# Kernel tuning notes

Measured on AMD Instinct MI355X. Metric: run time of the kernel, lower is better.

Reference implementation:

```python
import jax, jax.numpy as jnp
import numpy as np


def pairwise_distance(x):
    # x: [B,N,F] -> squared euclidean distance matrix [B,N,N]
    sq = jnp.sum(x * x, axis=-1)
    d = sq[:, :, None] + sq[:, None, :] - 2.0 * jnp.einsum('bnd,bmd->bnm', x, x)
    return jnp.maximum(d, 0.0)


def knn_adjacency(dist, k):
    # keep the k nearest neighbors of each point (binary adjacency)
    B, N, _ = dist.shape
    idx = jax.lax.top_k(-dist, k)[1]  # [B,N,k]
    A = jnp.zeros((B, N, N), dist.dtype)
    return A.at[jnp.arange(B)[:, None, None], jnp.arange(N)[None, :, None], idx].set(1.0)


def get_laplacian(A):
    # normalized graph Laplacian L = I - D^{-1/2} A D^{-1/2}
    d = jnp.sum(A, axis=-1)
    dinv = jnp.where(d > 0, 1.0 / jnp.sqrt(jnp.maximum(d, 1e-12)), 0.0)
    An = A * dinv[:, :, None] * dinv[:, None, :]
    return jnp.eye(A.shape[-1], dtype=A.dtype)[None] - An


def cheb_conv(x, L, W, b, K):
    # DenseChebConv: Chebyshev recurrence T0=x, T1=Lx, Tk=2L T_{k-1}-T_{k-2};
    # concat along features then dense projection. x:[B,N,Fin], W:[K*Fin,Fout]
    xs = [x]
    if K > 1:
        xs.append(jnp.einsum('bnm,bmf->bnf', L, x))
    for _ in range(2, K):
        xs.append(2.0 * jnp.einsum('bnm,bmf->bnf', L, xs[-1]) - xs[-2])
    xk = jnp.concatenate(xs, axis=-1)
    return jnp.einsum('bnf,fo->bno', xk, W) + b


def segment_max(out, idx):
    # fused replacement of the per-batch/per-cluster python loops:
    # out:[B,N,F], idx:[B,R,S] -> max-pooled cluster features [B,R,F]
    B = out.shape[0]
    g = out[jnp.arange(B)[:, None, None], idx]  # [B,R,S,F]
    return jnp.max(g, axis=2)


def setup_inputs():
    key = jax.random.key(0)
    ks = jax.random.split(key, 12)
    B, N, R, S, P = 32, 1024, 64, 16, 55
    inp = {}
    inp['x'] = jax.random.normal(ks[0], (B, N, 7), jnp.float32)
    inp['x2'] = jax.random.normal(ks[1], (B, N, 3), jnp.float32)
    inp['laplacian_Reeb'] = jax.random.normal(ks[2], (B, R, R), jnp.float32)
    inp['W1'] = jax.random.normal(ks[3], (3 * 7, 64), jnp.float32) * 0.1
    inp['b1'] = jnp.zeros((64,), jnp.float32)
    inp['W_reeb'] = jax.random.normal(ks[4], (6 * 64, 256), jnp.float32) * 0.05
    inp['b_reeb'] = jnp.zeros((256,), jnp.float32)
    inp['W_fps'] = jax.random.normal(ks[5], (6 * 64, 256), jnp.float32) * 0.05
    inp['b_fps'] = jnp.zeros((256,), jnp.float32)
    inp['fc1_w'] = jax.random.normal(ks[6], (512, 256), jnp.float32) * 0.05
    inp['fc1_b'] = jnp.zeros((256,), jnp.float32)
    inp['fc3_w'] = jax.random.normal(ks[7], (256, 40), jnp.float32) * 0.05
    inp['fc3_b'] = jnp.zeros((40,), jnp.float32)
    inp['sccs'] = jax.random.randint(ks[8], (B, R, S), 0, N)
    inp['sccs_fps'] = jax.random.randint(ks[9], (B, P, N), 0, N)
    inp['k'] = 30
    inp['batch_size'] = B
    inp['num_points'] = N
    return inp


def reference(x, x2, laplacian_Reeb, W1, b1, W_reeb, b_reeb, W_fps, b_fps,
              fc1_w, fc1_b, fc3_w, fc3_b, sccs, sccs_fps, k, batch_size, num_points):
    sg = jax.lax.stop_gradient
    # point-cloud kNN Laplacian (torch.no_grad in original)
    L = sg(get_laplacian(knn_adjacency(pairwise_distance(x), k)))
    out = jax.nn.relu(cheb_conv(x, L, W1, b1, 3))  # [B,N,64]
    reg1 = jnp.sum(jnp.einsum('bnf,bnm,bmg->bfg', out, L, out) ** 2)
    # Reeb-graph segment max pooling (no_grad in original)
    V_reeb = sg(segment_max(out, sccs))  # [B,R,64]
    L_reeb = sg(laplacian_Reeb)
    out_reeb = jax.nn.relu(cheb_conv(V_reeb, L_reeb, W_reeb, b_reeb, 6))  # [B,R,256]
    reg2 = jnp.sum(jnp.einsum('bnf,bnm,bmg->bfg', out_reeb, L_reeb, out_reeb) ** 2)
    # FPS cluster max pooling (no_grad in original)
    V_fps = sg(segment_max(out, sccs_fps))  # [B,55,64]
    L_fps = sg(get_laplacian(pairwise_distance(V_fps)))
    out_fps = jax.nn.relu(cheb_conv(V_fps, L_fps, W_fps, b_fps, 6))  # [B,55,256]
    reg3 = jnp.sum(jnp.einsum('bnf,bnm,bmg->bfg', out_fps, L_fps, out_fps) ** 2)
    feat = jnp.concatenate([jnp.max(out_reeb, axis=1), jnp.max(out_fps, axis=1)], axis=1)  # [B,512]
    h = jax.nn.relu(feat @ fc1_w + fc1_b)
    logits = h @ fc3_w + fc3_b  # [B,40]
    regs = jnp.stack([reg1, reg2, reg3,
                      jnp.sum(fc1_w[:, 0] ** 2), fc1_b[0] ** 2,
                      jnp.sum(fc3_w[:, 0] ** 2), fc3_b[0] ** 2])
    return logits, regs
```

## Files before the change

### kernel.cpp

```cpp
#include <hip/hip_runtime.h>
#include <math.h>

#define BN 32
#define NP 1024
#define KNN 30
#define NR 64
#define NFPS 55

__device__ __forceinline__ float lap_s() {
    const float dv = 1.0f / sqrtf(30.0f);
    return dv * dv;
}

__device__ __forceinline__ float dist7(const float4& xiA, const float4& xiB,
                                       float sqi, const float4& ca, const float4& cb) {
#pragma clang fp contract(off)
    float dot = xiA.x * ca.x;
    dot = fmaf(xiA.y, ca.y, dot);
    dot = fmaf(xiA.z, ca.z, dot);
    dot = fmaf(xiA.w, ca.w, dot);
    dot = fmaf(xiB.x, cb.x, dot);
    dot = fmaf(xiB.y, cb.y, dot);
    dot = fmaf(xiB.z, cb.z, dot);
    float r = sqi + cb.w;
    r = r - 2.f * dot;
    return fmaxf(r, 0.f);
}

__global__ __launch_bounds__(256) void k_knn(const float* __restrict__ x,
                                             int* __restrict__ knn,
                                             float* __restrict__ xs1) {
    __shared__ float xls[NP * 8];
    __shared__ float vals[4 * KNN * 64];
    __shared__ float Tm[4 * 64];
    __shared__ int   Pk[4 * 64];
    int b = blockIdx.x;
    int t = threadIdx.x;
    int ln = t & 63, wv = t >> 6;

    const float* xb = x + (size_t)b * NP * 7;
    for (int q = t; q < NP * 8; q += 256) {
        int r = q >> 3, d = q & 7;
        xls[q] = (d < 7) ? xb[r * 7 + d] : 0.f;
    }
    __syncthreads();
    for (int r = t; r < NP; r += 256) {
        float s = 0.f;
#pragma unroll
        for (int d = 0; d < 7; ++d) { float v = xls[r * 8 + d]; s += v * v; }
        xls[r * 8 + 7] = s;
    }
    __syncthreads();

    int grow = blockIdx.y * 64 + ln;
    float4 xiA = *(const float4*)&xls[grow * 8];
    float4 xiB = *(const float4*)&xls[grow * 8 + 4];
    float sqi = xiB.w;

    float bd[KNN];
#pragma unroll
    for (int q = 0; q < KNN; ++q) bd[q] = __builtin_inff();
    int jbase = wv * 256;
    for (int jc = 0; jc < 256; jc += 4) {
        const float* p = &xls[(jbase + jc) * 8];
        float4 a0 = *(const float4*)(p +  0), b0 = *(const float4*)(p +  4);
        float4 a1 = *(const float4*)(p +  8), b1 = *(const float4*)(p + 12);
        float4 a2 = *(const float4*)(p + 16), b2 = *(const float4*)(p + 20);
        float4 a3 = *(const float4*)(p + 24), b3 = *(const float4*)(p + 28);
        float d0 = dist7(xiA, xiB, sqi, a0, b0);
        float d1 = dist7(xiA, xiB, sqi, a1, b1);
        float d2 = dist7(xiA, xiB, sqi, a2, b2);
        float d3 = dist7(xiA, xiB, sqi, a3, b3);
#pragma unroll
        for (int q = KNN - 1; q >= 1; --q) bd[q] = __builtin_amdgcn_fmed3f(bd[q - 1], d0, bd[q]);
        bd[0] = fminf(bd[0], d0);
#pragma unroll
        for (int q = KNN - 1; q >= 1; --q) bd[q] = __builtin_amdgcn_fmed3f(bd[q - 1], d1, bd[q]);
        bd[0] = fminf(bd[0], d1);
#pragma unroll
        for (int q = KNN - 1; q >= 1; --q) bd[q] = __builtin_amdgcn_fmed3f(bd[q - 1], d2, bd[q]);
        bd[0] = fminf(bd[0], d2);
#pragma unroll
        for (int q = KNN - 1; q >= 1; --q) bd[q] = __builtin_amdgcn_fmed3f(bd[q - 1], d3, bd[q]);
        bd[0] = fminf(bd[0], d3);
    }
#pragma unroll
    for (int q = 0; q < KNN; ++q) vals[wv * (KNN * 64) + q * 64 + ln] = bd[q];
    __syncthreads();

    if (t < 64) {
        const float inf = __builtin_inff();
        float h0 = vals[0 * 1920 + t], n0v = vals[0 * 1920 + 64 + t];
        float h1 = vals[1 * 1920 + t], n1v = vals[1 * 1920 + 64 + t];
        float h2 = vals[2 * 1920 + t], n2v = vals[2 * 1920 + 64 + t];
        float h3 = vals[3 * 1920 + t], n3v = vals[3 * 1920 + 64 + t];
        int p0 = 0, p1 = 0, p2 = 0, p3 = 0;
        float lv0 = inf, lv1 = inf, lv2 = inf, lv3 = inf;
        int r0 = 0, r1 = 0, r2 = 0, r3 = 0;
        for (int s = 0; s < KNN; ++s) {
            float best = h0; int bw = 0;
            if (h1 < best) { best = h1; bw = 1; }
            if (h2 < best) { best = h2; bw = 2; }
            if (h3 < best) { best = h3; bw = 3; }
            if (bw == 0) {
                r0 = (best == lv0) ? r0 + 1 : 1; lv0 = best;
                ++p0; h0 = n0v; n0v = (p0 + 1 < KNN) ? vals[0 * 1920 + (p0 + 1) * 64 + t] : inf;
            } else if (bw == 1) {
                r1 = (best == lv1) ? r1 + 1 : 1; lv1 = best;
                ++p1; h1 = n1v; n1v = (p1 + 1 < KNN) ? vals[1 * 1920 + (p1 + 1) * 64 + t] : inf;
            } else if (bw == 2) {
                r2 = (best == lv2) ? r2 + 1 : 1; lv2 = best;
                ++p2; h2 = n2v; n2v = (p2 + 1 < KNN) ? vals[2 * 1920 + (p2 + 1) * 64 + t] : inf;
            } else {
                r3 = (best == lv3) ? r3 + 1 : 1; lv3 = best;
                ++p3; h3 = n3v; n3v = (p3 + 1 < KNN) ? vals[3 * 1920 + (p3 + 1) * 64 + t] : inf;
            }
        }
        Tm[0 * 64 + t] = lv0; Pk[0 * 64 + t] = 0 | (r0 << 8) | (p0 << 16);
        int bacc = p0;
        Tm[1 * 64 + t] = lv1; Pk[1 * 64 + t] = bacc | (r1 << 8) | (p1 << 16); bacc += p1;
        Tm[2 * 64 + t] = lv2; Pk[2 * 64 + t] = bacc | (r2 << 8) | (p2 << 16); bacc += p2;
        Tm[3 * 64 + t] = lv3; Pk[3 * 64 + t] = bacc | (r3 << 8) | (p3 << 16);
    }
    __syncthreads();

    float Tw = Tm[wv * 64 + ln];
    int pk = Pk[wv * 64 + ln];
    int base = pk & 255, need = (pk >> 8) & 255, tk = pk >> 16;
    int* kout = knn + ((size_t)b * NP + grow) * KNN;
    float n0 = 0.f, n1 = 0.f, n2 = 0.f, n3 = 0.f, n4 = 0.f, n5 = 0.f, n6 = 0.f;
    int cs = 0, ct = 0;
    for (int jc = 0; jc < 256; jc += 4) {
        const float* p = &xls[(jbase + jc) * 8];
        float4 a0 = *(const float4*)(p +  0), b0 = *(const float4*)(p +  4);
        float4 a1 = *(const float4*)(p +  8), b1 = *(const float4*)(p + 12);
        float4 a2 = *(const float4*)(p + 16), b2 = *(const float4*)(p + 20);
        float4 a3 = *(const float4*)(p + 24), b3 = *(const float4*)(p + 28);
        float d0 = dist7(xiA, xiB, sqi, a0, b0);
        float d1 = dist7(xiA, xiB, sqi, a1, b1);
        float d2 = dist7(xiA, xiB, sqi, a2, b2);
        float d3 = dist7(xiA, xiB, sqi, a3, b3);
#pragma unroll
        for (int u = 0; u < 4; ++u) {
            float dist = (u == 0) ? d0 : (u == 1) ? d1 : (u == 2) ? d2 : d3;
            const float4& ca = (u == 0) ? a0 : (u == 1) ? a1 : (u == 2) ? a2 : a3;
            const float4& cb = (u == 0) ? b0 : (u == 1) ? b1 : (u == 2) ? b2 : b3;
            bool lt = dist < Tw;
            bool eq = (dist == Tw) && (ct < need);
            if ((lt || eq) && (cs + ct < tk)) {
                kout[base + cs + ct] = jbase + jc + u;
                cs += lt ? 1 : 0;
                ct += eq ? 1 : 0;
                n0 += ca.x; n1 += ca.y; n2 += ca.z; n3 += ca.w;
                n4 += cb.x; n5 += cb.y; n6 += cb.z;
            }
        }
    }
    for (int q = cs + ct; q < tk; ++q) kout[base + q] = grow;
    float* nsb = vals;
    nsb[wv * 448 + 0 * 64 + ln] = n0;
    nsb[wv * 448 + 1 * 64 + ln] = n1;
    nsb[wv * 448 + 2 * 64 + ln] = n2;
    nsb[wv * 448 + 3 * 64 + ln] = n3;
    nsb[wv * 448 + 4 * 64 + ln] = n4;
    nsb[wv * 448 + 5 * 64 + ln] = n5;
    nsb[wv * 448 + 6 * 64 + ln] = n6;
    __syncthreads();
    for (int u = t; u < 448; u += 256) {
        int d = u >> 6, rl = u & 63;
        float tot = nsb[d * 64 + rl] + nsb[448 + d * 64 + rl]
                  + nsb[896 + d * 64 + rl] + nsb[1344 + d * 64 + rl];
        int gr = blockIdx.y * 64 + rl;
        xs1[((size_t)b * NP + gr) * 7 + d] = xls[gr * 8 + d] - lap_s() * tot;
    }
}

__global__ __launch_bounds__(256) void k_out(const float* __restrict__ x,
                                             const float* __restrict__ xs1,
                                             const int* __restrict__ knn,
                                             const float* __restrict__ W1,
                                             const float* __restrict__ b1,
                                             float* __restrict__ out,
                                             const float* __restrict__ fc1_w,
                                             const float* __restrict__ fc1_b,
                                             const float* __restrict__ fc3_w,
                                             const float* __restrict__ fc3_b,
                                             float* __restrict__ regs) {
    __shared__ float x1s[NP * 7];
    __shared__ float x0s[64 * 7];
    __shared__ float fr[64 * 21];
    __shared__ float W1s[21 * 64];
    __shared__ float b1s[64];
    int b = blockIdx.x, y = blockIdx.y;
    int t = threadIdx.x;
    if (y == 16) {
        if (b != 0) return;
        float* r1 = x1s;
        float* r2 = x1s + 256;
        float s1 = 0.f;
        for (int i = t; i < 512; i += 256) { float v = fc1_w[(size_t)i * 256]; s1 += v * v; }
        float v2 = fc3_w[(size_t)t * 40];
        r1[t] = s1; r2[t] = v2 * v2;
        __syncthreads();
        for (int st = 128; st > 0; st >>= 1) {
            if (t < st) { r1[t] += r1[t + st]; r2[t] += r2[t + st]; }
            __syncthreads();
        }
        if (t == 0) {
            regs[0] = 0.f; regs[1] = 0.f; regs[2] = 0.f;
            regs[3] = r1[0];
            regs[4] = fc1_b[0] * fc1_b[0];
            regs[5] = r2[0];
            regs[6] = fc3_b[0] * fc3_b[0];
        }
        return;
    }
    int rbase = y * 64;
    for (int q = t; q < NP * 7; q += 256) x1s[q] = xs1[(size_t)b * NP * 7 + q];
    for (int q = t; q < 64 * 7; q += 256) x0s[q] = x[(size_t)b * NP * 7 + (size_t)rbase * 7 + q];
    for (int q = t; q < 21 * 64; q += 256) W1s[q] = W1[q];
    if (t < 64) b1s[t] = b1[t];
    __syncthreads();
    if (t < 64) {
        int i = rbase + t;
        float f[21];
#pragma unroll
        for (int d = 0; d < 7; ++d) { f[d] = x0s[t * 7 + d]; f[7 + d] = x1s[i * 7 + d]; }
        float ns[7] = {0.f, 0.f, 0.f, 0.f, 0.f, 0.f, 0.f};
        const int* kn = knn + ((size_t)b * NP + i) * KNN;
        for (int q = 0; q < KNN; ++q) {
            int j = kn[q];
#pragma unroll
            for (int d = 0; d < 7; ++d) ns[d] += x1s[j * 7 + d];
        }
        const float s = lap_s();
#pragma unroll
        for (int d = 0; d < 7; ++d) f[14 + d] = 2.f * (f[7 + d] - s * ns[d]) - f[d];
#pragma unroll
        for (int d = 0; d < 21; ++d) fr[t * 21 + d] = f[d];
    }
    __syncthreads();
    int o = t & 63, g = t >> 6;
    for (int m = 0; m < 16; ++m) {
        int r = g * 16 + m;
        float acc = b1s[o];
#pragma unroll
        for (int d = 0; d < 21; ++d) acc += fr[r * 21 + d] * W1s[d * 64 + o];
        out[((size_t)b * NP + rbase + r) * 64 + o] = fmaxf(acc, 0.f);
    }
}

__global__ __launch_bounds__(256) void k_z1v(const float* __restrict__ out,
                                             const int* __restrict__ knn,
                                             const int* __restrict__ sccs,
                                             const int* __restrict__ sccs_fps,
                                             float* __restrict__ Z1,
                                             float* __restrict__ Vr,
                                             float* __restrict__ Vf) {
    __shared__ int idxs[1024];
    __shared__ float red[256];
    int b = blockIdx.x, y = blockIdx.y;
    int t = threadIdx.x;
    const float* ob = out + (size_t)b * NP * 64;
    if (y < 256) {
        int i = y * 4 + (t >> 6);
        int f = t & 63;
        const int* kn = knn + ((size_t)b * NP + i) * KNN;
        float sum = 0.f;
        for (int q = 0; q < KNN; ++q) sum += ob[(size_t)kn[q] * 64 + f];
        Z1[((size_t)b * NP + i) * 64 + f] = ob[(size_t)i * 64 + f] - lap_s() * sum;
    } else if (y < 272) {
        int r = (y - 256) * 4 + (t >> 6);
        int f = t & 63;
        const int* sc = sccs + ((size_t)b * NR + r) * 16;
        float m = -__builtin_inff();
        for (int q = 0; q < 16; ++q) m = fmaxf(m, ob[(size_t)sc[q] * 64 + f]);
        Vr[((size_t)b * NR + r) * 64 + f] = m;
    } else {
        int p = y - 272;
        const int* sp = sccs_fps + ((size_t)b * NFPS + p) * 1024;
        for (int q = t; q < 1024; q += 256) idxs[q] = sp[q];
        __syncthreads();
        int f = t & 63, sc = t >> 6;
        float m = -__builtin_inff();
        for (int s = sc; s < 1024; s += 4) m = fmaxf(m, ob[(size_t)idxs[s] * 64 + f]);
        red[t] = m; __syncthreads();
        if (sc == 0) {
            m = fmaxf(fmaxf(red[f], red[64 + f]), fmaxf(red[128 + f], red[192 + f]));
            Vf[((size_t)b * NFPS + p) * 64 + f] = m;
        }
    }
}

__device__ __forceinline__ void t1_impl(const float* __restrict__ out,
                                        const float* __restrict__ Z1,
                                        float* __restrict__ regs,
                                        float* buf, int y) {
    int b = blockIdx.x;
    int t = threadIdx.x;
    float* os = buf;
    float* zs = buf + 4096;
    float* red = buf + 8192;
    int f0 = y * 32;
    int fl = t >> 3;
    int gb = (t & 7) * 8;
    float acc[8];
#pragma unroll
    for (int q = 0; q < 8; ++q) acc[q] = 0.f;
    for (int c = 0; c < 16; ++c) {
        const float* ob = out + ((size_t)b * NP + c * 64) * 64;
        const float* zb = Z1 + ((size_t)b * NP + c * 64) * 64;
        for (int q = t; q < 64 * 64; q += 256) { os[q] = ob[q]; zs[q] = zb[q]; }
        __syncthreads();
        for (int n = 0; n < 64; ++n) {
            float a = os[n * 64 + f0 + fl];
#pragma unroll
            for (int q = 0; q < 8; ++q) acc[q] += a * zs[n * 64 + gb + q];
        }
        __syncthreads();
    }
    float loc = 0.f;
#pragma unroll
    for (int q = 0; q < 8; ++q) loc += acc[q] * acc[q];
    red[t] = loc; __syncthreads();
    for (int st = 128; st > 0; st >>= 1) { if (t < st) red[t] += red[t + st]; __syncthreads(); }
    if (t == 0) atomicAdd(&regs[0], red[0]);
}

__device__ __forceinline__ void lfps_impl(const float* __restrict__ Vfps,
                                          float* __restrict__ Lf, float* buf) {
    int b = blockIdx.x;
    int t = threadIdx.x;
    float* Vs = buf;
    float* sq = buf + 3520;
    float* dist = buf + 3584;
    float* dinv = buf + 6609;
    for (int q = t; q < NFPS * 64; q += 256) Vs[q] = Vfps[(size_t)b * NFPS * 64 + q];
    __syncthreads();
    if (t < NFPS) {
        float s = 0.f;
        for (int f = 0; f < 64; ++f) { float v = Vs[t * 64 + f]; s += v * v; }
        sq[t] = s;
    }
    __syncthreads();
    for (int q = t; q < NFPS * NFPS; q += 256) {
        int i = q / NFPS, j = q % NFPS;
        float dot = 0.f;
        for (int f = 0; f < 64; ++f) dot += Vs[i * 64 + f] * Vs[j * 64 + f];
        dist[q] = fmaxf(sq[i] + sq[j] - 2.f * dot, 0.f);
    }
    __syncthreads();
    if (t < NFPS) {
        float s = 0.f;
        for (int j = 0; j < NFPS; ++j) s += dist[t * NFPS + j];
        dinv[t] = (s > 0.f) ? 1.0f / sqrtf(fmaxf(s, 1e-12f)) : 0.f;
    }
    __syncthreads();
    for (int q = t; q < NFPS * NFPS; q += 256) {
        int i = q / NFPS, j = q % NFPS;
        Lf[(size_t)b * NFPS * NFPS + q] = ((i == j) ? 1.f : 0.f) - dist[q] * dinv[i] * dinv[j];
    }
}

template<int N>
__device__ __forceinline__ void cheb_impl(const float* __restrict__ L,
                                          const float* __restrict__ V,
                                          const float* __restrict__ W,
                                          const float* __restrict__ bias,
                                          float* __restrict__ out,
                                          float* __restrict__ Z,
                                          float* Ls, float* bA, float* bB, float* Ws,
                                          int b, int sl) {
    constexpr int NPAD = (N + 3) & ~3;
    int t = threadIdx.x;
    int c0 = (t & 15) * 4;
    int r0 = (t >> 4) * 4;

    for (int q = t; q < 64 * 64; q += 256) { Ls[q] = 0.f; bA[q] = 0.f; bB[q] = 0.f; }
    __syncthreads();
    for (int q = t; q < N * N; q += 256) {
        int r = q / N, m = q % N;
        Ls[r * 64 + m] = L[(size_t)b * N * N + q];
    }
    for (int q = t; q < N * 64; q += 256) bA[q] = V[(size_t)b * N * 64 + q];
    {
        const float* Wk = W + sl * 64;
        for (int q = t; q < 64 * 64; q += 256) Ws[q] = Wk[(q >> 6) * 256 + (q & 63)];
    }
    float4 a4[4];
    {
        float4 bv = *(const float4*)&bias[sl * 64 + c0];
#pragma unroll
        for (int i = 0; i < 4; ++i) a4[i] = bv;
    }
    __syncthreads();

    auto accum = [&](const float* xb) {
#pragma unroll 2
        for (int m = 0; m < 64; m += 4) {
            float4 xv[4], wv[4];
#pragma unroll
            for (int i = 0; i < 4; ++i) xv[i] = *(const float4*)&xb[(r0 + i) * 64 + m];
#pragma unroll
            for (int mm = 0; mm < 4; ++mm) wv[mm] = *(const float4*)&Ws[(m + mm) * 64 + c0];
#pragma unroll
            for (int i = 0; i < 4; ++i) {
                float xi0 = xv[i].x, xi1 = xv[i].y, xi2 = xv[i].z, xi3 = xv[i].w;
                a4[i].x += xi0 * wv[0].x; a4[i].y += xi0 * wv[0].y; a4[i].z += xi0 * wv[0].z; a4[i].w += xi0 * wv[0].w;
                a4[i].x += xi1 * wv[1].x; a4[i].y += xi1 * wv[1].y; a4[i].z += xi1 * wv[1].z; a4[i].w += xi1 * wv[1].w;
                a4[i].x += xi2 * wv[2].x; a4[i].y += xi2 * wv[2].y; a4[i].z += xi2 * wv[2].z; a4[i].w += xi2 * wv[2].w;
                a4[i].x += xi3 * wv[3].x; a4[i].y += xi3 * wv[3].y; a4[i].z += xi3 * wv[3].z; a4[i].w += xi3 * wv[3].w;
            }
        }
    };
    auto chebmm = [&](const float* src, float* dst, bool first) {
        float4 acc[4];
#pragma unroll
        for (int i = 0; i < 4; ++i) acc[i] = make_float4(0.f, 0.f, 0.f, 0.f);
#pragma unroll 2
        for (int m = 0; m < NPAD; m += 4) {
            float4 sv[4], lv[4];
#pragma unroll
            for (int mm = 0; mm < 4; ++mm) sv[mm] = *(const float4*)&src[(m + mm) * 64 + c0];
#pragma unroll
            for (int i = 0; i < 4; ++i) lv[i] = *(const float4*)&Ls[(r0 + i) * 64 + m];
#pragma unroll
            for (int i = 0; i < 4; ++i) {
                float l0 = lv[i].x, l1 = lv[i].y, l2 = lv[i].z, l3 = lv[i].w;
                acc[i].x += l0 * sv[0].x; acc[i].y += l0 * sv[0].y; acc[i].z += l0 * sv[0].z; acc[i].w += l0 * sv[0].w;
                acc[i].x += l1 * sv[1].x; acc[i].y += l1 * sv[1].y; acc[i].z += l1 * sv[1].z; acc[i].w += l1 * sv[1].w;
                acc[i].x += l2 * sv[2].x; acc[i].y += l2 * sv[2].y; acc[i].z += l2 * sv[2].z; acc[i].w += l2 * sv[2].w;
                acc[i].x += l3 * sv[3].x; acc[i].y += l3 * sv[3].y; acc[i].z += l3 * sv[3].z; acc[i].w += l3 * sv[3].w;
            }
        }
#pragma unroll
        for (int i = 0; i < 4; ++i) {
            if (r0 + i < N) {
                float4* d = (float4*)&dst[(r0 + i) * 64 + c0];
                if (first) *d = acc[i];
                else {
                    float4 od = *d;
                    *d = make_float4(2.f * acc[i].x - od.x, 2.f * acc[i].y - od.y,
                                     2.f * acc[i].z - od.z, 2.f * acc[i].w - od.w);
                }
            }
        }
    };
    auto loadW = [&](int k) {
        const float* Wk = W + (size_t)k * 64 * 256 + sl * 64;
        for (int q = t; q < 64 * 64; q += 256) Ws[q] = Wk[(q >> 6) * 256 + (q & 63)];
    };

    accum(bA);                 __syncthreads();
    chebmm(bA, bB, true);      loadW(1);  __syncthreads();
    accum(bB);                 __syncthreads();
    chebmm(bB, bA, false);     loadW(2);  __syncthreads();
    accum(bA);                 __syncthreads();
    chebmm(bA, bB, false);     loadW(3);  __syncthreads();
    accum(bB);                 __syncthreads();
    chebmm(bB, bA, false);     loadW(4);  __syncthreads();
    accum(bA);                 __syncthreads();
    chebmm(bA, bB, false);     loadW(5);  __syncthreads();
    accum(bB);                 __syncthreads();

    float* ob = out + (size_t)b * N * 256 + sl * 64;
#pragma unroll
    for (int i = 0; i < 4; ++i) {
        if (r0 + i < N) {
            float4 v = make_float4(fmaxf(a4[i].x, 0.f), fmaxf(a4[i].y, 0.f),
                                   fmaxf(a4[i].z, 0.f), fmaxf(a4[i].w, 0.f));
            *(float4*)&bA[(r0 + i) * 64 + c0] = v;
            *(float4*)&ob[(size_t)(r0 + i) * 256 + c0] = v;
        }
    }
    __syncthreads();
    {
        float4 acc[4];
#pragma unroll
        for (int i = 0; i < 4; ++i) acc[i] = make_float4(0.f, 0.f, 0.f, 0.f);
#pragma unroll 2
        for (int m = 0; m < NPAD; m += 4) {
            float4 sv[4], lv[4];
#pragma unroll
            for (int mm = 0; mm < 4; ++mm) sv[mm] = *(const float4*)&bA[(m + mm) * 64 + c0];
#pragma unroll
            for (int i = 0; i < 4; ++i) lv[i] = *(const float4*)&Ls[(r0 + i) * 64 + m];
#pragma unroll
            for (int i = 0; i < 4; ++i) {
                float l0 = lv[i].x, l1 = lv[i].y, l2 = lv[i].z, l3 = lv[i].w;
                acc[i].x += l0 * sv[0].x; acc[i].y += l0 * sv[0].y; acc[i].z += l0 * sv[0].z; acc[i].w += l0 * sv[0].w;
                acc[i].x += l1 * sv[1].x; acc[i].y += l1 * sv[1].y; acc[i].z += l1 * sv[1].z; acc[i].w += l1 * sv[1].w;
                acc[i].x += l2 * sv[2].x; acc[i].y += l2 * sv[2].y; acc[i].z += l2 * sv[2].z; acc[i].w += l2 * sv[2].w;
                acc[i].x += l3 * sv[3].x; acc[i].y += l3 * sv[3].y; acc[i].z += l3 * sv[3].z; acc[i].w += l3 * sv[3].w;
            }
        }
        float* zb = Z + (size_t)b * N * 256 + sl * 64;
#pragma unroll
        for (int i = 0; i < 4; ++i)
            if (r0 + i < N) *(float4*)&zb[(size_t)(r0 + i) * 256 + c0] = acc[i];
    }
}

template<int N>
__device__ __forceinline__ void treg_impl(const float* __restrict__ out,
                                          const float* __restrict__ Z,
                                          float* __restrict__ reg,
                                          float* zs, float* os, float* red, int y) {
    int b = blockIdx.x;
    int f0 = (y >> 1) * 32;
    int g0 = (y & 1) * 128;
    int t = threadIdx.x;
    for (int q = t; q < N * 128; q += 256) {
        int r = q >> 7, gl = q & 127;
        zs[q] = Z[(size_t)b * N * 256 + r * 256 + g0 + gl];
    }
    for (int q = t; q < N * 32; q += 256) {
        int r = q >> 5, f = q & 31;
        os[q] = out[(size_t)b * N * 256 + r * 256 + f0 + f];
    }
    __syncthreads();
    int fl = t >> 3;
    int gb = (t & 7) * 16;
    float accv[16];
#pragma unroll
    for (int q = 0; q < 16; ++q) accv[q] = 0.f;
    for (int n = 0; n < N; ++n) {
        float a = os[n * 32 + fl];
        const float* zr = zs + n * 128 + gb;
#pragma unroll
        for (int q = 0; q < 16; ++q) accv[q] += a * zr[q];
    }
    float loc = 0.f;
#pragma unroll
    for (int q = 0; q < 16; ++q) loc += accv[q] * accv[q];
    red[t] = loc; __syncthreads();
    for (int st = 128; st > 0; st >>= 1) { if (t < st) red[t] += red[t + st]; __syncthreads(); }
    if (t == 0) atomicAdd(reg, red[0]);
}

__global__ __launch_bounds__(256) void k_mid1(
        const float* __restrict__ out, const float* __restrict__ Z1,
        const float* __restrict__ Vfps, float* __restrict__ regs,
        float* __restrict__ Lf,
        const float* __restrict__ Lr, const float* __restrict__ Vr,
        const float* __restrict__ Wr, const float* __restrict__ br,
        float* __restrict__ outR, float* __restrict__ Zr) {
    __shared__ float smem[16384];
    int y = blockIdx.y;
    if (y < 2)       t1_impl(out, Z1, regs, smem, y);
    else if (y == 2) lfps_impl(Vfps, Lf, smem);
    else cheb_impl<NR>(Lr, Vr, Wr, br, outR, Zr,
                       smem, smem + 4096, smem + 8192, smem + 12288,
                       blockIdx.x, y - 3);
}

__global__ __launch_bounds__(256) void k_mid2(
        const float* __restrict__ Lf, const float* __restrict__ Vf,
        const float* __restrict__ Wf, const float* __restrict__ bf,
        float* __restrict__ outP, float* __restrict__ Zf,
        const float* __restrict__ outR, const float* __restrict__ Zr,
        float* __restrict__ regs) {
    __shared__ float smem[16384];
    int y = blockIdx.y;
    if (y < 4) cheb_impl<NFPS>(Lf, Vf, Wf, bf, outP, Zf,
                               smem, smem + 4096, smem + 8192, smem + 12288,
                               blockIdx.x, y);
    else treg_impl<NR>(outR, Zr, regs + 1, smem, smem + 8192, smem + 10240, y - 4);
}

__global__ __launch_bounds__(256) void k_fin(
        const float* __restrict__ outP, const float* __restrict__ Zf,
        const float* __restrict__ outR,
        const float* __restrict__ fc1_w, const float* __restrict__ fc1_b,
        const float* __restrict__ fc3_w, const float* __restrict__ fc3_b,
        float* __restrict__ regs, float* __restrict__ logits) {
    __shared__ float smem[10496];
    int y = blockIdx.y;
    if (y < 16) treg_impl<NFPS>(outP, Zf, regs + 2, smem, smem + 8192, smem + 10240, y);
    else {
        int b = blockIdx.x, t = threadIdx.x;
        float* feat = smem;
        float* h = smem + 8192;
        float m = -__builtin_inff();
        for (int r = 0; r < NR; ++r) m = fmaxf(m, outR[((size_t)b * NR + r) * 256 + t]);
        feat[t] = m;
        m = -__builtin_inff();
        for (int p = 0; p < NFPS; ++p) m = fmaxf(m, outP[((size_t)b * NFPS + p) * 256 + t]);
        feat[256 + t] = m;
        __syncthreads();
        float a = fc1_b[t];
        for (int i = 0; i < 512; ++i) a += feat[i] * fc1_w[(size_t)i * 256 + t];
        h[t] = fmaxf(a, 0.f);
        __syncthreads();
        if (t < 40) {
            float a2 = fc3_b[t];
            for (int i = 0; i < 256; ++i) a2 += h[i] * fc3_w[(size_t)i * 40 + t];
            logits[(size_t)b * 40 + t] = a2;
        }
    }
}

extern "C" void kernel_launch(void* const* d_in, const int* in_sizes, int n_in,
                              void* d_out, int out_size, void* d_ws, size_t ws_size,
                              hipStream_t stream) {
    const float* x      = (const float*)d_in[0];
    const float* L_reeb = (const float*)d_in[2];
    const float* W1     = (const float*)d_in[3];
    const float* b1     = (const float*)d_in[4];
    const float* W_reeb = (const float*)d_in[5];
    const float* b_reeb = (const float*)d_in[6];
    const float* W_fps  = (const float*)d_in[7];
    const float* b_fps  = (const float*)d_in[8];
    const float* fc1_w  = (const float*)d_in[9];
    const float* fc1_b  = (const float*)d_in[10];
    const float* fc3_w  = (const float*)d_in[11];
    const float* fc3_b  = (const float*)d_in[12];
    const int*   sccs   = (const int*)d_in[13];
    const int*   sccs_f = (const int*)d_in[14];

    float* outv = (float*)d_out;
    float* regs = outv + 1280;

    char* w = (char*)d_ws;
    size_t off = 0;
    auto alloc = [&](size_t bytes) { void* p = w + off; off = (off + bytes + 255) & ~(size_t)255; return p; };
    int*   knn   = (int*)  alloc((size_t)BN * NP * KNN * 4);
    float* xs1   = (float*)alloc((size_t)BN * NP * 7 * 4);
    float* outF  = (float*)alloc((size_t)BN * NP * 64 * 4);
    float* Z1    = (float*)alloc((size_t)BN * NP * 64 * 4);
    float* Vreeb = (float*)alloc((size_t)BN * NR * 64 * 4);
    float* outRb = (float*)alloc((size_t)BN * NR * 256 * 4);
    float* Z2    = (float*)alloc((size_t)BN * NR * 256 * 4);
    float* Vfps  = (float*)alloc((size_t)BN * NFPS * 64 * 4);
    float* Lfps  = (float*)alloc((size_t)BN * NFPS * NFPS * 4);
    float* outP  = (float*)alloc((size_t)BN * NFPS * 256 * 4);
    float* Z3    = (float*)alloc((size_t)BN * NFPS * 256 * 4);

    k_knn<<<dim3(BN, NP / 64), 256, 0, stream>>>(x, knn, xs1);
    k_out<<<dim3(BN, 17), 256, 0, stream>>>(x, xs1, knn, W1, b1, outF,
                                            fc1_w, fc1_b, fc3_w, fc3_b, regs);
    k_z1v<<<dim3(BN, 256 + 16 + NFPS), 256, 0, stream>>>(outF, knn, sccs, sccs_f,
                                                         Z1, Vreeb, Vfps);
    k_mid1<<<dim3(BN, 7), 256, 0, stream>>>(outF, Z1, Vfps, regs, Lfps,
                                            L_reeb, Vreeb, W_reeb, b_reeb, outRb, Z2);
    k_mid2<<<dim3(BN, 20), 256, 0, stream>>>(Lfps, Vfps, W_fps, b_fps, outP, Z3,
                                             outRb, Z2, regs);
    k_fin<<<dim3(BN, 17), 256, 0, stream>>>(outP, Z3, outRb,
                                            fc1_w, fc1_b, fc3_w, fc3_b, regs, outv);
}
```

Baseline: 385.3 us.

## Split reg1 Gram computation over node chunks with atomic partials; bitmap-dedupe FPS gather

The reg1 term out^T·Z1 per batch was computed by only 2 blocks per batch, each walking all 1024 nodes serially. It is now split into 8 node-chunk blocks per batch that compute a 4x4 register-tiled partial 64x64 product and atomically add it into a zeroed global buffer. A later block squares and sums that buffer. The FPS cluster max-pool also builds a shared-memory bitmap of member indices, so each unique row is gathered once instead of once per duplicate index. This adds global atomics, an extra buffer, and a reduction stage, and it makes the float summation order nondeterministic.

```diff
diff --git a/kernel.cpp b/kernel.cpp
--- a/kernel.cpp
+++ b/kernel.cpp
@@ -185,7 +185,8 @@
                                              const float* __restrict__ fc1_b,
                                              const float* __restrict__ fc3_w,
                                              const float* __restrict__ fc3_b,
-                                             float* __restrict__ regs) {
+                                             float* __restrict__ regs,
+                                             float* __restrict__ Cbuf) {
     __shared__ float x1s[NP * 7];
     __shared__ float x0s[64 * 7];
     __shared__ float fr[64 * 21];
@@ -194,6 +195,8 @@
     int b = blockIdx.x, y = blockIdx.y;
     int t = threadIdx.x;
     if (y == 16) {
+        float* cb = Cbuf + (size_t)b * 4096;
+        for (int q = t; q < 4096; q += 256) cb[q] = 0.f;
         if (b != 0) return;
         float* r1 = x1s;
         float* r2 = x1s + 256;
@@ -257,7 +260,7 @@
                                              float* __restrict__ Z1,
                                              float* __restrict__ Vr,
                                              float* __restrict__ Vf) {
-    __shared__ int idxs[1024];
+    __shared__ unsigned bmw[32];
     __shared__ float red[256];
     int b = blockIdx.x, y = blockIdx.y;
     int t = threadIdx.x;
@@ -279,11 +282,23 @@
     } else {
         int p = y - 272;
         const int* sp = sccs_fps + ((size_t)b * NFPS + p) * 1024;
-        for (int q = t; q < 1024; q += 256) idxs[q] = sp[q];
+        if (t < 32) bmw[t] = 0u;
+        __syncthreads();
+        for (int q = t; q < 1024; q += 256) {
+            int r = sp[q];
+            atomicOr(&bmw[r >> 5], 1u << (r & 31));
+        }
         __syncthreads();
         int f = t & 63, sc = t >> 6;
         float m = -__builtin_inff();
-        for (int s = sc; s < 1024; s += 4) m = fmaxf(m, ob[(size_t)idxs[s] * 64 + f]);
+        for (int w0 = sc * 8; w0 < sc * 8 + 8; ++w0) {
+            unsigned w = bmw[w0];
+            while (w) {
+                int bit = __ffs(w) - 1;
+                w &= w - 1;
+                m = fmaxf(m, ob[(size_t)(w0 * 32 + bit) * 64 + f]);
+            }
+        }
         red[t] = m; __syncthreads();
         if (sc == 0) {
             m = fmaxf(fmaxf(red[f], red[64 + f]), fmaxf(red[128 + f], red[192 + f]));
@@ -292,39 +307,46 @@
     }
 }
 
-__device__ __forceinline__ void t1_impl(const float* __restrict__ out,
+__device__ __forceinline__ void t1_part(const float* __restrict__ out,
                                         const float* __restrict__ Z1,
-                                        float* __restrict__ regs,
+                                        float* __restrict__ Cbuf,
                                         float* buf, int y) {
-    int b = blockIdx.x;
-    int t = threadIdx.x;
+    int b = blockIdx.x, t = threadIdx.x;
     float* os = buf;
-    float* zs = buf + 4096;
-    float* red = buf + 8192;
-    int f0 = y * 32;
-    int fl = t >> 3;
-    int gb = (t & 7) * 8;
-    float acc[8];
-#pragma unroll
-    for (int q = 0; q < 8; ++q) acc[q] = 0.f;
-    for (int c = 0; c < 16; ++c) {
-        const float* ob = out + ((size_t)b * NP + c * 64) * 64;
-        const float* zb = Z1 + ((size_t)b * NP + c * 64) * 64;
-        for (int q = t; q < 64 * 64; q += 256) { os[q] = ob[q]; zs[q] = zb[q]; }
-        __syncthreads();
-        for (int n = 0; n < 64; ++n) {
-            float a = os[n * 64 + f0 + fl];
-#pragma unroll
-            for (int q = 0; q < 8; ++q) acc[q] += a * zs[n * 64 + gb + q];
-        }
-        __syncthreads();
-    }
-    float loc = 0.f;
-#pragma unroll
-    for (int q = 0; q < 8; ++q) loc += acc[q] * acc[q];
-    red[t] = loc; __syncthreads();
-    for (int st = 128; st > 0; st >>= 1) { if (t < st) red[t] += red[t + st]; __syncthreads(); }
-    if (t == 0) atomicAdd(&regs[0], red[0]);
+    float* zs = buf + 8192;
+    const float* ob = out + ((size_t)b * NP + (size_t)y * 128) * 64;
+    const float* zb = Z1 + ((size_t)b * NP + (size_t)y * 128) * 64;
+    for (int q = t; q < 128 * 64; q += 256) { os[q] = ob[q]; zs[q] = zb[q]; }
+    __syncthreads();
+    int f0 = (t & 15) * 4, g0 = (t >> 4) * 4;
+    float4 ac0 = make_float4(0.f, 0.f, 0.f, 0.f);
+    float4 ac1 = ac0, ac2 = ac0, ac3 = ac0;
+#pragma unroll 4
+    for (int n = 0; n < 128; ++n) {
+        float4 ov = *(const float4*)&os[n * 64 + f0];
+        float4 zv = *(const float4*)&zs[n * 64 + g0];
+        ac0.x += ov.x * zv.x; ac0.y += ov.x * zv.y; ac0.z += ov.x * zv.z; ac0.w += ov.x * zv.w;
+        ac1.x += ov.y * zv.x; ac1.y += ov.y * zv.y; ac1.z += ov.y * zv.z; ac1.w += ov.y * zv.w;
+        ac2.x += ov.z * zv.x; ac2.y += ov.z * zv.y; ac2.z += ov.z * zv.z; ac2.w += ov.z * zv.w;
+        ac3.x += ov.w * zv.x; ac3.y += ov.w * zv.y; ac3.z += ov.w * zv.z; ac3.w += ov.w * zv.w;
+    }
+    float* cb = Cbuf + (size_t)b * 4096;
+    atomicAdd(&cb[(f0 + 0) * 64 + g0 + 0], ac0.x);
+    atomicAdd(&cb[(f0 + 0) * 64 + g0 + 1], ac0.y);
+    atomicAdd(&cb[(f0 + 0) * 64 + g0 + 2], ac0.z);
+    atomicAdd(&cb[(f0 + 0) * 64 + g0 + 3], ac0.w);
+    atomicAdd(&cb[(f0 + 1) * 64 + g0 + 0], ac1.x);
+    atomicAdd(&cb[(f0 + 1) * 64 + g0 + 1], ac1.y);
+    atomicAdd(&cb[(f0 + 1) * 64 + g0 + 2], ac1.z);
+    atomicAdd(&cb[(f0 + 1) * 64 + g0 + 3], ac1.w);
+    atomicAdd(&cb[(f0 + 2) * 64 + g0 + 0], ac2.x);
+    atomicAdd(&cb[(f0 + 2) * 64 + g0 + 1], ac2.y);
+    atomicAdd(&cb[(f0 + 2) * 64 + g0 + 2], ac2.z);
+    atomicAdd(&cb[(f0 + 2) * 64 + g0 + 3], ac2.w);
+    atomicAdd(&cb[(f0 + 3) * 64 + g0 + 0], ac3.x);
+    atomicAdd(&cb[(f0 + 3) * 64 + g0 + 1], ac3.y);
+    atomicAdd(&cb[(f0 + 3) * 64 + g0 + 2], ac3.z);
+    atomicAdd(&cb[(f0 + 3) * 64 + g0 + 3], ac3.w);
 }
 
 __device__ __forceinline__ void lfps_impl(const float* __restrict__ Vfps,
@@ -540,18 +562,18 @@
 
 __global__ __launch_bounds__(256) void k_mid1(
         const float* __restrict__ out, const float* __restrict__ Z1,
-        const float* __restrict__ Vfps, float* __restrict__ regs,
+        const float* __restrict__ Vfps, float* __restrict__ Cbuf,
         float* __restrict__ Lf,
         const float* __restrict__ Lr, const float* __restrict__ Vr,
         const float* __restrict__ Wr, const float* __restrict__ br,
         float* __restrict__ outR, float* __restrict__ Zr) {
     __shared__ float smem[16384];
     int y = blockIdx.y;
-    if (y < 2)       t1_impl(out, Z1, regs, smem, y);
-    else if (y == 2) lfps_impl(Vfps, Lf, smem);
+    if (y < 8)       t1_part(out, Z1, Cbuf, smem, y);
+    else if (y == 8) lfps_impl(Vfps, Lf, smem);
     else cheb_impl<NR>(Lr, Vr, Wr, br, outR, Zr,
                        smem, smem + 4096, smem + 8192, smem + 12288,
-                       blockIdx.x, y - 3);
+                       blockIdx.x, y - 9);
 }
 
 __global__ __launch_bounds__(256) void k_mid2(
@@ -559,13 +581,22 @@
         const float* __restrict__ Wf, const float* __restrict__ bf,
         float* __restrict__ outP, float* __restrict__ Zf,
         const float* __restrict__ outR, const float* __restrict__ Zr,
-        float* __restrict__ regs) {
+        const float* __restrict__ Cbuf, float* __restrict__ regs) {
     __shared__ float smem[16384];
     int y = blockIdx.y;
     if (y < 4) cheb_impl<NFPS>(Lf, Vf, Wf, bf, outP, Zf,
                                smem, smem + 4096, smem + 8192, smem + 12288,
                                blockIdx.x, y);
-    else treg_impl<NR>(outR, Zr, regs + 1, smem, smem + 8192, smem + 10240, y - 4);
+    else if (y < 20) treg_impl<NR>(outR, Zr, regs + 1, smem, smem + 8192, smem + 10240, y - 4);
+    else {
+        int b = blockIdx.x, t = threadIdx.x;
+        float* red = smem;
+        float loc = 0.f;
+        for (int q = t; q < 4096; q += 256) { float v = Cbuf[(size_t)b * 4096 + q]; loc += v * v; }
+        red[t] = loc; __syncthreads();
+        for (int st = 128; st > 0; st >>= 1) { if (t < st) red[t] += red[t + st]; __syncthreads(); }
+        if (t == 0) atomicAdd(&regs[0], red[0]);
+    }
 }
 
 __global__ __launch_bounds__(256) void k_fin(
@@ -635,16 +666,17 @@
     float* Lfps  = (float*)alloc((size_t)BN * NFPS * NFPS * 4);
     float* outP  = (float*)alloc((size_t)BN * NFPS * 256 * 4);
     float* Z3    = (float*)alloc((size_t)BN * NFPS * 256 * 4);
+    float* Cbuf  = (float*)alloc((size_t)BN * 4096 * 4);
 
     k_knn<<<dim3(BN, NP / 64), 256, 0, stream>>>(x, knn, xs1);
     k_out<<<dim3(BN, 17), 256, 0, stream>>>(x, xs1, knn, W1, b1, outF,
-                                            fc1_w, fc1_b, fc3_w, fc3_b, regs);
+                                            fc1_w, fc1_b, fc3_w, fc3_b, regs, Cbuf);
     k_z1v<<<dim3(BN, 256 + 16 + NFPS), 256, 0, stream>>>(outF, knn, sccs, sccs_f,
                                                          Z1, Vreeb, Vfps);
-    k_mid1<<<dim3(BN, 7), 256, 0, stream>>>(outF, Z1, Vfps, regs, Lfps,
-                                            L_reeb, Vreeb, W_reeb, b_reeb, outRb, Z2);
-    k_mid2<<<dim3(BN, 20), 256, 0, stream>>>(Lfps, Vfps, W_fps, b_fps, outP, Z3,
-                                             outRb, Z2, regs);
+    k_mid1<<<dim3(BN, 13), 256, 0, stream>>>(outF, Z1, Vfps, Cbuf, Lfps,
+                                             L_reeb, Vreeb, W_reeb, b_reeb, outRb, Z2);
+    k_mid2<<<dim3(BN, 21), 256, 0, stream>>>(Lfps, Vfps, W_fps, b_fps, outP, Z3,
+                                             outRb, Z2, Cbuf, regs);
     k_fin<<<dim3(BN, 17), 256, 0, stream>>>(outP, Z3, outRb,
                                             fc1_w, fc1_b, fc3_w, fc3_b, regs, outv);
 }
```

Measured after the change: 362.5 us. -5.9%, faster.
